# Kernel tuning notes

Hardware: AMD Instinct MI355X
Metric: run time of the kernel (lower is better)

The kernel has to match this reference:

```python
import jax, jax.numpy as jnp
import numpy as np
import math

B, S, D, H = 2, 2048, 1024, 16
DQ = D // H  # d_qkv = 64


def setup_inputs() -> dict:
    key = jax.random.key(0)
    k1, k2, k3, k4 = jax.random.split(key, 4)
    return {
        "Q": jax.random.normal(k1, (B, S, D), dtype=jnp.float32),
        "K": jax.random.normal(k2, (B, S, D), dtype=jnp.float32),
        "V": jax.random.normal(k3, (B, S, D), dtype=jnp.float32),
        "Wo_w": jax.random.normal(k4, (D, D), dtype=jnp.float32) * 0.02,
        "Wo_b": jnp.zeros((D,), dtype=jnp.float32),
        "mask": 1,
    }


def reference(Q, K, V, Wo_w, Wo_b, mask):
    # Note: original module defines Wq/Wk/Wv but never applies them in forward.
    q = Q.reshape(B, S, H, DQ)
    k = K.reshape(B, S, H, DQ)
    v = V.reshape(B, S, H, DQ)
    # raw QK^T scores: [B, H, S, S]
    scores = jnp.einsum("bqhd,bkhd->bhqk", q, k)
    if mask:
        # torch.triu_indices(S, S) default offset=0 -> mask where key >= query
        # (diagonal included). Fill applied BEFORE the sqrt(d) scaling, as in source.
        tri = jnp.arange(S)[:, None] <= jnp.arange(S)[None, :]  # [S, S]
        scores = jnp.where(tri, jnp.float32(-1e9), scores)
    scale = scores / math.sqrt(DQ)
    attn = jax.nn.softmax(scale, axis=-1)
    ctx = jnp.einsum("bhqk,bkhd->bqhd", attn, v).reshape(B, S, D)
    return ctx @ Wo_w.T + Wo_b
```

## Files before the change

kernel.cpp:

```cpp
#include <hip/hip_runtime.h>
#include <hip/hip_bf16.h>
#include <stdint.h>

#define B_  2
#define S_  2048
#define D_  1024
#define H_  16
#define DQ_ 64
#define QT_ (S_/64)

#define C1_ 0.18033688011112042f

typedef float f32x4  __attribute__((ext_vector_type(4)));
typedef float f32x16 __attribute__((ext_vector_type(16)));
typedef short bf16x8 __attribute__((ext_vector_type(8)));

__device__ __forceinline__ unsigned short f2bf(float f) {
    uint32_t u = __float_as_uint(f);
    u += 0x7fffu + ((u >> 16) & 1u);
    return (unsigned short)(u >> 16);
}
__device__ __forceinline__ float bf2f(unsigned short u) {
    return __uint_as_float(((uint32_t)u) << 16);
}
__device__ __forceinline__ float fast_exp2(float x) {
#if __has_builtin(__builtin_amdgcn_exp2f)
    return __builtin_amdgcn_exp2f(x);
#else
    float r; asm("v_exp_f32 %0, %1" : "=v"(r) : "v"(x)); return r;
#endif
}
__device__ __forceinline__ uint32_t cvt_pk_bf16(float lo, float hi) {
    uint32_t r;
    asm("v_cvt_pk_bf16_f32 %0, %1, %2" : "=v"(r) : "v"(lo), "v"(hi));
    return r;
}
__device__ __forceinline__ void permlane32_swap(uint32_t &a, uint32_t &b) {
    asm volatile("v_permlane32_swap_b32 %0, %1" : "+v"(a), "+v"(b));
}

__global__ __launch_bounds__(256) void prep_kernel(
    const float* __restrict__ K, const float* __restrict__ V,
    const float* __restrict__ W,
    unsigned short* __restrict__ Kf, unsigned short* __restrict__ Vf,
    unsigned short* __restrict__ Wb, float* __restrict__ Pv)
{
    __shared__ unsigned short Ls[64][72];
    __shared__ float Pp[8][64];
    const int blk = blockIdx.x, tid = threadIdx.x;

    if (blk < 2048) {
        const bool isV = blk < 1024;
        const int gb = isV ? blk : (blk - 1024);
        const int g = gb >> 5, j = gb & 31;
        const int b = g >> 4, h = g & 15;
        const float* src0 = (isV ? V : K) + ((size_t)(b*S_ + j*64))*D_ + h*64;

        {
            int row = tid >> 2, col0 = (tid & 3) * 16;
            const float* src = src0 + (size_t)row*D_ + col0;
            float4 f0 = ((const float4*)src)[0];
            float4 f1 = ((const float4*)src)[1];
            float4 f2 = ((const float4*)src)[2];
            float4 f3 = ((const float4*)src)[3];
            unsigned short* d = &Ls[row][col0];
            d[0]=f2bf(f0.x); d[1]=f2bf(f0.y); d[2]=f2bf(f0.z); d[3]=f2bf(f0.w);
            d[4]=f2bf(f1.x); d[5]=f2bf(f1.y); d[6]=f2bf(f1.z); d[7]=f2bf(f1.w);
            d[8]=f2bf(f2.x); d[9]=f2bf(f2.y); d[10]=f2bf(f2.z); d[11]=f2bf(f2.w);
            d[12]=f2bf(f3.x); d[13]=f2bf(f3.y); d[14]=f2bf(f3.z); d[15]=f2bf(f3.w);
        }
        __syncthreads();

        if (isV) {
            #pragma unroll
            for (int ps = 0; ps < 2; ++ps) {
                const int slot = tid + ps*256;
                const int fb = slot >> 6, l = slot & 63;
                const int s = fb >> 1, kk = fb & 1;
                const int hi = l >> 5, l31 = l & 31;
                const int dcol = kk*32 + l31;
                unsigned short us[8];
                float p = 0.f;
                #pragma unroll
                for (int r = 0; r < 8; ++r) {
                    unsigned short u = Ls[s*16 + hi*8 + r][dcol];
                    us[r] = u;
                    p += bf2f(u);
                }
                *(uint4*)(Vf + ((size_t)gb*8 + fb)*512 + (size_t)l*8) = *(uint4*)us;
                Pp[s*2 + hi][dcol] = p;
            }
            __syncthreads();
            if (tid < 64) {
                float t = 0.f;
                #pragma unroll
                for (int i = 0; i < 8; ++i) t += Pp[i][tid];
                Pv[((size_t)g*64 + tid)*32 + j] = t;
            }
        } else {
            #pragma unroll
            for (int ps = 0; ps < 2; ++ps) {
                const int slot = tid + ps*256;
                const int fb = slot >> 6, l = slot & 63;
                const int wk = fb >> 2, s = fb & 3;
                const int hi = l >> 5, l31 = l & 31;
                uint4 val = *(const uint4*)&Ls[wk*32 + l31][s*16 + hi*8];
                *(uint4*)(Kf + ((size_t)gb*8 + fb)*512 + (size_t)l*8) = val;
            }
        }
    } else {
        int i = (blk - 2048)*256 + tid;
        float4 f = ((const float4*)W)[i];
        ushort4 o;
        o.x = f2bf(f.x); o.y = f2bf(f.y); o.z = f2bf(f.z); o.w = f2bf(f.w);
        ((ushort4*)Wb)[i] = o;
    }
}

__global__ __launch_bounds__(256, 2) void attn_kernel(
    const float* __restrict__ Q,
    const unsigned short* __restrict__ Kf,
    const unsigned short* __restrict__ Vf,
    const float* __restrict__ Pv,
    unsigned short* __restrict__ ctx,
    const int* __restrict__ maskp)
{
    __shared__ union {
        unsigned short qs[64][72];
        struct { float osum[2][32][68]; float lsum[2][32]; } red;
    } sm;

    const int bid = blockIdx.x;
    const int g = bid & 31;
    const int p = bid >> 5;
    const int qt = (p < 8) ? p : (p < 16) ? 23 - p : (p < 24) ? p : 55 - p;
    const int h = g & 15, b = g >> 4;
    const int tid  = threadIdx.x;
    const int wave = tid >> 6, lane = tid & 63;
    const int wq = wave >> 1, wk = wave & 1;
    const int hi = lane >> 5, l31 = lane & 31;
    const int maskv = maskp[0];

    if (maskv && qt == 0 && tid < 64) {
        const float* pv = Pv + ((size_t)g*64 + tid)*32;
        float s = 0.f;
        #pragma unroll
        for (int i = 0; i < 32; ++i) s += pv[i];
        ctx[(size_t)b*S_*D_ + h*64 + tid] = f2bf(s * (1.0f/S_));
    }

    {
        const int row = tid >> 2, col0 = (tid & 3) * 16;
        const float* src = Q + ((size_t)(b*S_ + qt*64 + row))*D_ + h*64 + col0;
        float4 f0 = ((const float4*)src)[0];
        float4 f1 = ((const float4*)src)[1];
        float4 f2 = ((const float4*)src)[2];
        float4 f3 = ((const float4*)src)[3];
        unsigned short* d = &sm.qs[row][col0];
        d[0]=f2bf(f0.x*C1_); d[1]=f2bf(f0.y*C1_); d[2]=f2bf(f0.z*C1_); d[3]=f2bf(f0.w*C1_);
        d[4]=f2bf(f1.x*C1_); d[5]=f2bf(f1.y*C1_); d[6]=f2bf(f1.z*C1_); d[7]=f2bf(f1.w*C1_);
        d[8]=f2bf(f2.x*C1_); d[9]=f2bf(f2.y*C1_); d[10]=f2bf(f2.z*C1_); d[11]=f2bf(f2.w*C1_);
        d[12]=f2bf(f3.x*C1_); d[13]=f2bf(f3.y*C1_); d[14]=f2bf(f3.z*C1_); d[15]=f2bf(f3.w*C1_);
    }
    __syncthreads();
    bf16x8 qf[4];
    #pragma unroll
    for (int s = 0; s < 4; ++s)
        qf[s] = *(const bf16x8*)&sm.qs[wq*32 + l31][s*16 + hi*8];
    __syncthreads();

    const unsigned short* kfb =
        Kf + ((size_t)g*32*8 + wk*4)*512 + (size_t)lane*8;
    const unsigned short* vfb =
        Vf + ((size_t)g*32*8 + wk*4)*512 + (size_t)lane*8;

    int njw = maskv ? (qt + 1) : QT_;
    if (maskv && wq == 0 && wk == 1) njw = qt;

    f32x16 o[2] = {};
    float lsum = 0.f;

    bf16x8 ka[4], va[4], kb[4], vb[4];
    if (njw > 0) {
        #pragma unroll
        for (int s = 0; s < 4; ++s) {
            ka[s] = *(const bf16x8*)(kfb + s*512);
            va[s] = *(const bf16x8*)(vfb + s*512);
        }
    }
    if (njw > 1) {
        #pragma unroll
        for (int s = 0; s < 4; ++s) {
            kb[s] = *(const bf16x8*)(kfb + 4096 + s*512);
            vb[s] = *(const bf16x8*)(vfb + 4096 + s*512);
        }
    }

#define AITER(J, KC, VC)                                                      \
  {                                                                           \
    f32x16 st = {};                                                           \
    __builtin_amdgcn_s_setprio(1);                                            \
    st = __builtin_amdgcn_mfma_f32_32x32x16_bf16(KC[0], qf[0], st, 0,0,0);    \
    st = __builtin_amdgcn_mfma_f32_32x32x16_bf16(KC[1], qf[1], st, 0,0,0);    \
    st = __builtin_amdgcn_mfma_f32_32x32x16_bf16(KC[2], qf[2], st, 0,0,0);    \
    st = __builtin_amdgcn_mfma_f32_32x32x16_bf16(KC[3], qf[3], st, 0,0,0);    \
    __builtin_amdgcn_s_setprio(0);                                            \
    if ((J) + 2 < njw) {           \
      const unsigned short* kp_ = kfb + (size_t)((J)+2)*4096;                 \
      KC[0] = *(const bf16x8*)(kp_);                                          \
      KC[1] = *(const bf16x8*)(kp_ + 512);                                    \
      KC[2] = *(const bf16x8*)(kp_ + 1024);                                   \
      KC[3] = *(const bf16x8*)(kp_ + 1536);                                   \
    }                                                                         \
    float e[16];                                                              \
    const bool diag_ = maskv && ((J) == qt) && (wk == wq);                    \
    if (diag_) {                                                              \
      _Pragma("unroll")                                                       \
      for (int r = 0; r < 16; ++r) {                                          \
        int kr_ = (r&3) + 8*(r>>2) + 4*hi;                                    \
        float ev_ = fast_exp2(st[r]);                                         \
        e[r] = (kr_ >= l31) ? 0.f : ev_;                                      \
        lsum += e[r];                                                         \
      }                                                                       \
    } else {                                                                  \
      _Pragma("unroll")                                                       \
      for (int r = 0; r < 16; ++r) { e[r] = fast_exp2(st[r]); lsum += e[r]; } \
    }                                                                         \
    uint32_t p01_ = cvt_pk_bf16(e[0], e[1]),  p23_ = cvt_pk_bf16(e[2], e[3]); \
    uint32_t p45_ = cvt_pk_bf16(e[4], e[5]),  p67_ = cvt_pk_bf16(e[6], e[7]); \
    permlane32_swap(p01_, p45_); permlane32_swap(p23_, p67_);                 \
    uint32_t r01_ = cvt_pk_bf16(e[8], e[9]),  r23_ = cvt_pk_bf16(e[10], e[11]); \
    uint32_t r45_ = cvt_pk_bf16(e[12], e[13]), r67_ = cvt_pk_bf16(e[14], e[15]); \
    permlane32_swap(r01_, r45_); permlane32_swap(r23_, r67_);                 \
    union { uint32_t u[4]; bf16x8 v; } A0_, A1_;                              \
    A0_.u[0]=p01_; A0_.u[1]=p23_; A0_.u[2]=p45_; A0_.u[3]=p67_;               \
    A1_.u[0]=r01_; A1_.u[1]=r23_; A1_.u[2]=r45_; A1_.u[3]=r67_;               \
    __builtin_amdgcn_s_setprio(1);                                            \
    o[0] = __builtin_amdgcn_mfma_f32_32x32x16_bf16(A0_.v, VC[0], o[0], 0,0,0);\
    o[1] = __builtin_amdgcn_mfma_f32_32x32x16_bf16(A0_.v, VC[1], o[1], 0,0,0);\
    o[0] = __builtin_amdgcn_mfma_f32_32x32x16_bf16(A1_.v, VC[2], o[0], 0,0,0);\
    o[1] = __builtin_amdgcn_mfma_f32_32x32x16_bf16(A1_.v, VC[3], o[1], 0,0,0);\
    __builtin_amdgcn_s_setprio(0);                                            \
    if ((J) + 2 < njw) {           \
      const unsigned short* vp_ = vfb + (size_t)((J)+2)*4096;                 \
      VC[0] = *(const bf16x8*)(vp_);                                          \
      VC[1] = *(const bf16x8*)(vp_ + 512);                                    \
      VC[2] = *(const bf16x8*)(vp_ + 1024);                                   \
      VC[3] = *(const bf16x8*)(vp_ + 1536);                                   \
    }                                                                         \
  }

    int j = 0;
    for (; j + 1 < njw; j += 2) {
        AITER(j, ka, va);
        AITER(j+1, kb, vb);
    }
    if (j < njw) AITER(j, ka, va);
#undef AITER

    lsum += __shfl_xor(lsum, 32);

    if (wk == 1) {
        #pragma unroll
        for (int r = 0; r < 16; ++r) {
            int qr = (r&3) + 8*(r>>2) + 4*hi;
            sm.red.osum[wq][qr][l31]      = o[0][r];
            sm.red.osum[wq][qr][32 + l31] = o[1][r];
        }
        if (hi == 0) sm.red.lsum[wq][l31] = lsum;
    }
    __syncthreads();
    if (wk == 0) {
        float inv = 1.0f / (lsum + sm.red.lsum[wq][l31]);
        #pragma unroll
        for (int r = 0; r < 16; ++r) {
            int qr = (r&3) + 8*(r>>2) + 4*hi;
            float o0v = o[0][r] + sm.red.osum[wq][qr][l31];
            float o1v = o[1][r] + sm.red.osum[wq][qr][32 + l31];
            float invr = __shfl(inv, qr);
            int q = qt*64 + wq*32 + qr;
            if (!(maskv && q == 0)) {
                size_t base = ((size_t)(b*S_ + q))*D_ + h*64;
                ctx[base + l31]      = f2bf(o0v * invr);
                ctx[base + 32 + l31] = f2bf(o1v * invr);
            }
        }
    }
}

__global__ __launch_bounds__(256, 2) void proj_kernel(
    const unsigned short* __restrict__ A,
    const unsigned short* __restrict__ Bw,
    const float* __restrict__ bias,
    float* __restrict__ out)
{
    __shared__ unsigned short As[2][64][72];
    __shared__ unsigned short Bs[2][128][72];
    const int nt0 = blockIdx.x;
    const int mt0 = blockIdx.y;
    const int tid  = threadIdx.x;
    const int wave = tid >> 6, lane = tid & 63;
    const int quad = lane >> 4, ln = lane & 15;

    const int arow = tid >> 2, acol = (tid & 3)*16;
    const int brow = tid >> 1, bcol = (tid & 1)*32;
    const unsigned short* aptr = A  + ((size_t)(mt0*64  + arow)*1024 + acol);
    const unsigned short* bptr = Bw + ((size_t)(nt0*128 + brow)*1024 + bcol);

    uint4 a0 = ((const uint4*)aptr)[0], a1 = ((const uint4*)aptr)[1];
    uint4 b0 = ((const uint4*)bptr)[0], b1 = ((const uint4*)bptr)[1],
          b2 = ((const uint4*)bptr)[2], b3 = ((const uint4*)bptr)[3];

    f32x4 acc[4][2] = {};

    for (int kt = 0; kt < 16; ++kt) {
        const int cur = kt & 1;
        *((uint4*)&As[cur][arow][acol])    = a0;
        *((uint4*)&As[cur][arow][acol+8])  = a1;
        *((uint4*)&Bs[cur][brow][bcol])    = b0;
        *((uint4*)&Bs[cur][brow][bcol+8])  = b1;
        *((uint4*)&Bs[cur][brow][bcol+16]) = b2;
        *((uint4*)&Bs[cur][brow][bcol+24]) = b3;
        uint4 na0, na1, nb0, nb1, nb2, nb3;
        if (kt < 15) {
            const unsigned short* ap = aptr + (kt+1)*64;
            const unsigned short* bp = bptr + (kt+1)*64;
            na0 = ((const uint4*)ap)[0]; na1 = ((const uint4*)ap)[1];
            nb0 = ((const uint4*)bp)[0]; nb1 = ((const uint4*)bp)[1];
            nb2 = ((const uint4*)bp)[2]; nb3 = ((const uint4*)bp)[3];
        }
        __syncthreads();
        #pragma unroll
        for (int ks = 0; ks < 2; ++ks) {
            bf16x8 am[4], bn[2];
            #pragma unroll
            for (int i = 0; i < 4; ++i)
                am[i] = *(const bf16x8*)&As[cur][i*16 + ln][ks*32 + quad*8];
            #pragma unroll
            for (int i = 0; i < 2; ++i)
                bn[i] = *(const bf16x8*)&Bs[cur][wave*32 + i*16 + ln][ks*32 + quad*8];
            #pragma unroll
            for (int mi = 0; mi < 4; ++mi)
                #pragma unroll
                for (int ni = 0; ni < 2; ++ni)
                    acc[mi][ni] = __builtin_amdgcn_mfma_f32_16x16x32_bf16(
                        am[mi], bn[ni], acc[mi][ni], 0,0,0);
        }
        a0 = na0; a1 = na1;
        b0 = nb0; b1 = nb1; b2 = nb2; b3 = nb3;
    }

    #pragma unroll
    for (int mi = 0; mi < 4; ++mi)
        #pragma unroll
        for (int ni = 0; ni < 2; ++ni) {
            int row = mt0*64 + mi*16 + quad*4;
            int col = nt0*128 + wave*32 + ni*16 + ln;
            float bv = bias[col];
            #pragma unroll
            for (int r = 0; r < 4; ++r)
                out[(size_t)(row + r)*1024 + col] = acc[mi][ni][r] + bv;
        }
}

extern "C" void kernel_launch(void* const* d_in, const int* in_sizes, int n_in,
                              void* d_out, int out_size, void* d_ws, size_t ws_size,
                              hipStream_t stream)
{
    const float* Q   = (const float*)d_in[0];
    const float* K   = (const float*)d_in[1];
    const float* V   = (const float*)d_in[2];
    const float* Wo  = (const float*)d_in[3];
    const float* Wb  = (const float*)d_in[4];
    const int* maskp = (const int*)d_in[5];
    float* out = (float*)d_out;

    unsigned short* Kf   = (unsigned short*)d_ws;
    unsigned short* Vf   = Kf  + (size_t)B_*S_*D_;
    unsigned short* Wob  = Vf  + (size_t)B_*S_*D_;
    unsigned short* ctxb = Wob + (size_t)D_*D_;
    float* Pv = (float*)(ctxb + (size_t)B_*S_*D_);

    prep_kernel<<<3072, 256, 0, stream>>>(K, V, Wo, Kf, Vf, Wob, Pv);
    attn_kernel<<<1024, 256, 0, stream>>>(Q, Kf, Vf, Pv, ctxb, maskp);
    proj_kernel<<<dim3(8, 64), 256, 0, stream>>>(ctxb, Wob, Wb, out);
}
```

Baseline: 143.6 us.

## Have each attention wave cover both query halves to reuse K/V fragments

The attention block shrinks from four waves to two. Each wave now owns a 32-key column slice and computes both 32-row query halves with the same K/V register fragments, which halves K/V global fetches per block. On the diagonal tile, the masking and skip logic moves inside the iteration. The query-tile order changes to launch long causal tiles first, to reduce the tail. In exchange, each wave holds more accumulators and query fragments, and there are half as many waves in flight to hide latency.

```diff
diff --git a/kernel.cpp b/kernel.cpp
--- a/kernel.cpp
+++ b/kernel.cpp
@@ -14,6 +14,8 @@
 typedef float f32x4  __attribute__((ext_vector_type(4)));
 typedef float f32x16 __attribute__((ext_vector_type(16)));
 typedef short bf16x8 __attribute__((ext_vector_type(8)));
+
+#define MFMA32(A,B,C) __builtin_amdgcn_mfma_f32_32x32x16_bf16(A,B,C,0,0,0)
 
 __device__ __forceinline__ unsigned short f2bf(float f) {
     uint32_t u = __float_as_uint(f);
@@ -117,7 +119,7 @@
     }
 }
 
-__global__ __launch_bounds__(256, 2) void attn_kernel(
+__global__ __launch_bounds__(128, 2) void attn_kernel(
     const float* __restrict__ Q,
     const unsigned short* __restrict__ Kf,
     const unsigned short* __restrict__ Vf,
@@ -133,11 +135,11 @@
     const int bid = blockIdx.x;
     const int g = bid & 31;
     const int p = bid >> 5;
-    const int qt = (p < 8) ? p : (p < 16) ? 23 - p : (p < 24) ? p : 55 - p;
+    const int qt = (p < 8) ? 31 - p : (p < 16) ? p + 8 : (p < 24) ? 31 - p : p - 24;
     const int h = g & 15, b = g >> 4;
     const int tid  = threadIdx.x;
-    const int wave = tid >> 6, lane = tid & 63;
-    const int wq = wave >> 1, wk = wave & 1;
+    const int wk   = tid >> 6;
+    const int lane = tid & 63;
     const int hi = lane >> 5, l31 = lane & 31;
     const int maskv = maskp[0];
 
@@ -149,8 +151,10 @@
         ctx[(size_t)b*S_*D_ + h*64 + tid] = f2bf(s * (1.0f/S_));
     }
 
-    {
-        const int row = tid >> 2, col0 = (tid & 3) * 16;
+    #pragma unroll
+    for (int ps = 0; ps < 2; ++ps) {
+        const int slot = tid + ps*128;
+        const int row = slot >> 2, col0 = (slot & 3) * 16;
         const float* src = Q + ((size_t)(b*S_ + qt*64 + row))*D_ + h*64 + col0;
         float4 f0 = ((const float4*)src)[0];
         float4 f1 = ((const float4*)src)[1];
@@ -163,10 +167,12 @@
         d[12]=f2bf(f3.x*C1_); d[13]=f2bf(f3.y*C1_); d[14]=f2bf(f3.z*C1_); d[15]=f2bf(f3.w*C1_);
     }
     __syncthreads();
-    bf16x8 qf[4];
+    bf16x8 qfa[4], qfb[4];
     #pragma unroll
-    for (int s = 0; s < 4; ++s)
-        qf[s] = *(const bf16x8*)&sm.qs[wq*32 + l31][s*16 + hi*8];
+    for (int s = 0; s < 4; ++s) {
+        qfa[s] = *(const bf16x8*)&sm.qs[l31][s*16 + hi*8];
+        qfb[s] = *(const bf16x8*)&sm.qs[32 + l31][s*16 + hi*8];
+    }
     __syncthreads();
 
     const unsigned short* kfb =
@@ -174,11 +180,10 @@
     const unsigned short* vfb =
         Vf + ((size_t)g*32*8 + wk*4)*512 + (size_t)lane*8;
 
-    int njw = maskv ? (qt + 1) : QT_;
-    if (maskv && wq == 0 && wk == 1) njw = qt;
-
-    f32x16 o[2] = {};
-    float lsum = 0.f;
+    const int njw = maskv ? (qt + 1) : QT_;
+
+    f32x16 oa0 = {}, oa1 = {}, ob0 = {}, ob1 = {};
+    float lsa = 0.f, lsb = 0.f;
 
     bf16x8 ka[4], va[4], kb[4], vb[4];
     if (njw > 0) {
@@ -196,93 +201,139 @@
         }
     }
 
+#define PACK_PV(E, O0, O1, VC)                                                \
+    {                                                                         \
+      uint32_t p01_ = cvt_pk_bf16(E[0], E[1]),  p23_ = cvt_pk_bf16(E[2], E[3]); \
+      uint32_t p45_ = cvt_pk_bf16(E[4], E[5]),  p67_ = cvt_pk_bf16(E[6], E[7]); \
+      permlane32_swap(p01_, p45_); permlane32_swap(p23_, p67_);               \
+      uint32_t r01_ = cvt_pk_bf16(E[8], E[9]),  r23_ = cvt_pk_bf16(E[10], E[11]); \
+      uint32_t r45_ = cvt_pk_bf16(E[12], E[13]), r67_ = cvt_pk_bf16(E[14], E[15]); \
+      permlane32_swap(r01_, r45_); permlane32_swap(r23_, r67_);               \
+      union { uint32_t u[4]; bf16x8 v; } A0_, A1_;                            \
+      A0_.u[0]=p01_; A0_.u[1]=p23_; A0_.u[2]=p45_; A0_.u[3]=p67_;             \
+      A1_.u[0]=r01_; A1_.u[1]=r23_; A1_.u[2]=r45_; A1_.u[3]=r67_;             \
+      __builtin_amdgcn_s_setprio(1);                                          \
+      O0 = MFMA32(A0_.v, VC[0], O0);                                          \
+      O1 = MFMA32(A0_.v, VC[1], O1);                                          \
+      O0 = MFMA32(A1_.v, VC[2], O0);                                          \
+      O1 = MFMA32(A1_.v, VC[3], O1);                                          \
+      __builtin_amdgcn_s_setprio(0);                                          \
+    }
+
 #define AITER(J, KC, VC)                                                      \
   {                                                                           \
-    f32x16 st = {};                                                           \
-    __builtin_amdgcn_s_setprio(1);                                            \
-    st = __builtin_amdgcn_mfma_f32_32x32x16_bf16(KC[0], qf[0], st, 0,0,0);    \
-    st = __builtin_amdgcn_mfma_f32_32x32x16_bf16(KC[1], qf[1], st, 0,0,0);    \
-    st = __builtin_amdgcn_mfma_f32_32x32x16_bf16(KC[2], qf[2], st, 0,0,0);    \
-    st = __builtin_amdgcn_mfma_f32_32x32x16_bf16(KC[3], qf[3], st, 0,0,0);    \
-    __builtin_amdgcn_s_setprio(0);                                            \
-    if ((J) + 2 < njw) {           \
-      const unsigned short* kp_ = kfb + (size_t)((J)+2)*4096;                 \
-      KC[0] = *(const bf16x8*)(kp_);                                          \
-      KC[1] = *(const bf16x8*)(kp_ + 512);                                    \
-      KC[2] = *(const bf16x8*)(kp_ + 1024);                                   \
-      KC[3] = *(const bf16x8*)(kp_ + 1536);                                   \
+    const bool diagJ_ = maskv && ((J) == qt);                                 \
+      \
+    if (!(diagJ_ && wk == 1)) {                                               \
+      f32x16 st_ = {};                                                        \
+      __builtin_amdgcn_s_setprio(1);                                          \
+      st_ = MFMA32(KC[0], qfa[0], st_);                                       \
+      st_ = MFMA32(KC[1], qfa[1], st_);                                       \
+      st_ = MFMA32(KC[2], qfa[2], st_);                                       \
+      st_ = MFMA32(KC[3], qfa[3], st_);                                       \
+      __builtin_amdgcn_s_setprio(0);                                          \
+      float e[16];                                                            \
+      if (diagJ_) {                          \
+        _Pragma("unroll")                                                     \
+        for (int r = 0; r < 16; ++r) {                                        \
+          int kr_ = (r&3) + 8*(r>>2) + 4*hi;                                  \
+          float ev_ = fast_exp2(st_[r]);                                      \
+          e[r] = (kr_ >= l31) ? 0.f : ev_;                                    \
+          lsa += e[r];                                                        \
+        }                                                                     \
+      } else {                                                                \
+        _Pragma("unroll")                                                     \
+        for (int r = 0; r < 16; ++r) { e[r] = fast_exp2(st_[r]); lsa += e[r]; } \
+      }                                                                       \
+      PACK_PV(e, oa0, oa1, VC)                                                \
     }                                                                         \
-    float e[16];                                                              \
-    const bool diag_ = maskv && ((J) == qt) && (wk == wq);                    \
-    if (diag_) {                                                              \
-      _Pragma("unroll")                                                       \
-      for (int r = 0; r < 16; ++r) {                                          \
-        int kr_ = (r&3) + 8*(r>>2) + 4*hi;                                    \
-        float ev_ = fast_exp2(st[r]);                                         \
-        e[r] = (kr_ >= l31) ? 0.f : ev_;                                      \
-        lsum += e[r];                                                         \
+                                     \
+    {                                                                         \
+      f32x16 st_ = {};                                                        \
+      __builtin_amdgcn_s_setprio(1);                                          \
+      st_ = MFMA32(KC[0], qfb[0], st_);                                       \
+      st_ = MFMA32(KC[1], qfb[1], st_);                                       \
+      st_ = MFMA32(KC[2], qfb[2], st_);                                       \
+      st_ = MFMA32(KC[3], qfb[3], st_);                                       \
+      __builtin_amdgcn_s_setprio(0);                                          \
+      if ((J) + 2 < njw) {               \
+        const unsigned short* kp_ = kfb + (size_t)((J)+2)*4096;               \
+        KC[0] = *(const bf16x8*)(kp_);                                        \
+        KC[1] = *(const bf16x8*)(kp_ + 512);                                  \
+        KC[2] = *(const bf16x8*)(kp_ + 1024);                                 \
+        KC[3] = *(const bf16x8*)(kp_ + 1536);                                 \
       }                                                                       \
-    } else {                                                                  \
-      _Pragma("unroll")                                                       \
-      for (int r = 0; r < 16; ++r) { e[r] = fast_exp2(st[r]); lsum += e[r]; } \
-    }                                                                         \
-    uint32_t p01_ = cvt_pk_bf16(e[0], e[1]),  p23_ = cvt_pk_bf16(e[2], e[3]); \
-    uint32_t p45_ = cvt_pk_bf16(e[4], e[5]),  p67_ = cvt_pk_bf16(e[6], e[7]); \
-    permlane32_swap(p01_, p45_); permlane32_swap(p23_, p67_);                 \
-    uint32_t r01_ = cvt_pk_bf16(e[8], e[9]),  r23_ = cvt_pk_bf16(e[10], e[11]); \
-    uint32_t r45_ = cvt_pk_bf16(e[12], e[13]), r67_ = cvt_pk_bf16(e[14], e[15]); \
-    permlane32_swap(r01_, r45_); permlane32_swap(r23_, r67_);                 \
-    union { uint32_t u[4]; bf16x8 v; } A0_, A1_;                              \
-    A0_.u[0]=p01_; A0_.u[1]=p23_; A0_.u[2]=p45_; A0_.u[3]=p67_;               \
-    A1_.u[0]=r01_; A1_.u[1]=r23_; A1_.u[2]=r45_; A1_.u[3]=r67_;               \
-    __builtin_amdgcn_s_setprio(1);                                            \
-    o[0] = __builtin_amdgcn_mfma_f32_32x32x16_bf16(A0_.v, VC[0], o[0], 0,0,0);\
-    o[1] = __builtin_amdgcn_mfma_f32_32x32x16_bf16(A0_.v, VC[1], o[1], 0,0,0);\
-    o[0] = __builtin_amdgcn_mfma_f32_32x32x16_bf16(A1_.v, VC[2], o[0], 0,0,0);\
-    o[1] = __builtin_amdgcn_mfma_f32_32x32x16_bf16(A1_.v, VC[3], o[1], 0,0,0);\
-    __builtin_amdgcn_s_setprio(0);                                            \
-    if ((J) + 2 < njw) {           \
-      const unsigned short* vp_ = vfb + (size_t)((J)+2)*4096;                 \
-      VC[0] = *(const bf16x8*)(vp_);                                          \
-      VC[1] = *(const bf16x8*)(vp_ + 512);                                    \
-      VC[2] = *(const bf16x8*)(vp_ + 1024);                                   \
-      VC[3] = *(const bf16x8*)(vp_ + 1536);                                   \
+      float e[16];                                                            \
+      if (diagJ_ && wk == 1) {     \
+        _Pragma("unroll")                                                     \
+        for (int r = 0; r < 16; ++r) {                                        \
+          int kr_ = (r&3) + 8*(r>>2) + 4*hi;                                  \
+          float ev_ = fast_exp2(st_[r]);                                      \
+          e[r] = (kr_ >= l31) ? 0.f : ev_;                                    \
+          lsb += e[r];                                                        \
+        }                                                                     \
+      } else {                                                                \
+        _Pragma("unroll")                                                     \
+        for (int r = 0; r < 16; ++r) { e[r] = fast_exp2(st_[r]); lsb += e[r]; } \
+      }                                                                       \
+      PACK_PV(e, ob0, ob1, VC)                                                \
+      if ((J) + 2 < njw) {               \
+        const unsigned short* vp_ = vfb + (size_t)((J)+2)*4096;               \
+        VC[0] = *(const bf16x8*)(vp_);                                        \
+        VC[1] = *(const bf16x8*)(vp_ + 512);                                  \
+        VC[2] = *(const bf16x8*)(vp_ + 1024);                                 \
+        VC[3] = *(const bf16x8*)(vp_ + 1536);                                 \
+      }                                                                       \
     }                                                                         \
   }
 
     int j = 0;
     for (; j + 1 < njw; j += 2) {
-        AITER(j, ka, va);
+        AITER(j,   ka, va);
         AITER(j+1, kb, vb);
     }
     if (j < njw) AITER(j, ka, va);
 #undef AITER
-
-    lsum += __shfl_xor(lsum, 32);
+#undef PACK_PV
+
+    lsa += __shfl_xor(lsa, 32);
+    lsb += __shfl_xor(lsb, 32);
 
     if (wk == 1) {
         #pragma unroll
         for (int r = 0; r < 16; ++r) {
             int qr = (r&3) + 8*(r>>2) + 4*hi;
-            sm.red.osum[wq][qr][l31]      = o[0][r];
-            sm.red.osum[wq][qr][32 + l31] = o[1][r];
-        }
-        if (hi == 0) sm.red.lsum[wq][l31] = lsum;
+            sm.red.osum[0][qr][l31]      = oa0[r];
+            sm.red.osum[0][qr][32 + l31] = oa1[r];
+            sm.red.osum[1][qr][l31]      = ob0[r];
+            sm.red.osum[1][qr][32 + l31] = ob1[r];
+        }
+        if (hi == 0) { sm.red.lsum[0][l31] = lsa; sm.red.lsum[1][l31] = lsb; }
     }
     __syncthreads();
     if (wk == 0) {
-        float inv = 1.0f / (lsum + sm.red.lsum[wq][l31]);
+        float inva = 1.0f / (lsa + sm.red.lsum[0][l31]);
+        float invb = 1.0f / (lsb + sm.red.lsum[1][l31]);
         #pragma unroll
         for (int r = 0; r < 16; ++r) {
             int qr = (r&3) + 8*(r>>2) + 4*hi;
-            float o0v = o[0][r] + sm.red.osum[wq][qr][l31];
-            float o1v = o[1][r] + sm.red.osum[wq][qr][32 + l31];
-            float invr = __shfl(inv, qr);
-            int q = qt*64 + wq*32 + qr;
-            if (!(maskv && q == 0)) {
-                size_t base = ((size_t)(b*S_ + q))*D_ + h*64;
-                ctx[base + l31]      = f2bf(o0v * invr);
-                ctx[base + 32 + l31] = f2bf(o1v * invr);
+            float a0v = oa0[r] + sm.red.osum[0][qr][l31];
+            float a1v = oa1[r] + sm.red.osum[0][qr][32 + l31];
+            float b0v = ob0[r] + sm.red.osum[1][qr][l31];
+            float b1v = ob1[r] + sm.red.osum[1][qr][32 + l31];
+            float invra = __shfl(inva, qr);
+            float invrb = __shfl(invb, qr);
+            int qa = qt*64 + qr;
+            int qb = qt*64 + 32 + qr;
+            if (!(maskv && qa == 0)) {
+                size_t base = ((size_t)(b*S_ + qa))*D_ + h*64;
+                ctx[base + l31]      = f2bf(a0v * invra);
+                ctx[base + 32 + l31] = f2bf(a1v * invra);
+            }
+            {
+                size_t base = ((size_t)(b*S_ + qb))*D_ + h*64;
+                ctx[base + l31]      = f2bf(b0v * invrb);
+                ctx[base + 32 + l31] = f2bf(b1v * invrb);
             }
         }
     }
@@ -382,6 +433,6 @@
     float* Pv = (float*)(ctxb + (size_t)B_*S_*D_);
 
     prep_kernel<<<3072, 256, 0, stream>>>(K, V, Wo, Kf, Vf, Wob, Pv);
-    attn_kernel<<<1024, 256, 0, stream>>>(Q, Kf, Vf, Pv, ctxb, maskp);
+    attn_kernel<<<1024, 128, 0, stream>>>(Q, Kf, Vf, Pv, ctxb, maskp);
     proj_kernel<<<dim3(8, 64), 256, 0, stream>>>(ctxb, Wob, Wb, out);
 }
```

After: 146.5 us. 2.0% more time.
